# Optimization experiments

Measured on AMD Instinct MI355X. Metric: run time of the kernel, lower is better.

Reference implementation:

```python
import jax, jax.numpy as jnp
import numpy as np

B, T, D_IN, H = 256, 512, 64, 128
S_MIN, S_FRAC = 0.5, 0.5


def _gru_cell(x_i, h, W_ih, W_hh, b_ih, b_hh):
    # torch.nn.GRUCell semantics
    gi = x_i @ W_ih.T + b_ih          # [B, 3H]
    gh = h @ W_hh.T + b_hh            # [B, 3H]
    i_r, i_z, i_n = jnp.split(gi, 3, axis=-1)
    h_r, h_z, h_n = jnp.split(gh, 3, axis=-1)
    r = jax.nn.sigmoid(i_r + h_r)
    z = jax.nn.sigmoid(i_z + h_z)
    n = jnp.tanh(i_n + r * h_n)
    return (1.0 - z) * n + z * h


def _rk4_step(h, dt, W_node, b_node):
    # one fixed RK4 step of dh/dt = tanh(h @ W_node^T + b_node) over [t, t+dt]
    f = lambda hh: jnp.tanh(hh @ W_node.T + b_node)
    k1 = f(h)
    k2 = f(h + 0.5 * dt * k1)
    k3 = f(h + 0.5 * dt * k2)
    k4 = f(h + dt * k3)
    return h + (dt / 6.0) * (k1 + 2.0 * k2 + 2.0 * k3 + k4)


def setup_inputs() -> dict:
    key = jax.random.key(0)
    ks = jax.random.split(key, 8)
    x = jax.random.normal(ks[0], (B, T, D_IN), dtype=jnp.float32)
    # sorted per-sample time grid; all lens == T so argmax-longest picks row 0
    tp = jnp.broadcast_to(jnp.linspace(0.01, 1.0, T, dtype=jnp.float32), (B, T))
    # generate_samp_mask(x, s_min=0.5, s_frac=0.5), deterministic seed
    rng = np.random.default_rng(0)
    minimum_ind = int(T * S_MIN)
    extrap_ind = int(rng.integers(minimum_ind, T))
    n_inds = int(S_FRAC * extrap_ind)
    samp_inds = np.sort(rng.choice(np.arange(extrap_ind), n_inds, replace=False))
    mask_np = np.zeros(T, dtype=bool)
    mask_np[samp_inds] = True
    samp_mask = jnp.asarray(mask_np)
    s = 1.0 / np.sqrt(H)
    W_ih = jax.random.uniform(ks[1], (3 * H, D_IN), jnp.float32, -s, s)
    W_hh = jax.random.uniform(ks[2], (3 * H, H), jnp.float32, -s, s)
    b_ih = jax.random.uniform(ks[3], (3 * H,), jnp.float32, -s, s)
    b_hh = jax.random.uniform(ks[4], (3 * H,), jnp.float32, -s, s)
    W_node = jax.random.normal(ks[5], (H, H), jnp.float32) * 0.05
    b_node = jnp.zeros((H,), jnp.float32)
    W_out = jax.random.uniform(ks[6], (D_IN, H), jnp.float32, -s, s)
    b_out = jax.random.uniform(ks[7], (D_IN,), jnp.float32, -s, s)
    return {"x": x, "tp": tp, "samp_mask": samp_mask,
            "W_ih": W_ih, "W_hh": W_hh, "b_ih": b_ih, "b_hh": b_hh,
            "W_node": W_node, "b_node": b_node, "W_out": W_out, "b_out": b_out}


def reference(x, tp, samp_mask, W_ih, W_hh, b_ih, b_hh, W_node, b_node, W_out, b_out):
    # get_longest_tp: all lens equal -> row 0; prepend tp[0]-0.01
    t0 = tp[0]                                   # [T]
    ts = jnp.concatenate([t0[:1] - 0.01, t0])    # [T+1]
    dts = ts[1:] - ts[:-1]                       # [T]
    xs = jnp.transpose(x, (1, 0, 2))             # [T, B, D_in]
    h0 = jnp.zeros((x.shape[0], W_hh.shape[1]), x.dtype)

    def step(h, inp):
        dt, x_i, use_x = inp
        h_ode = _rk4_step(h, dt, W_node, b_node)
        prev_out = h @ W_out.T + b_out           # teacher-forcing from own output
        inp_vec = jnp.where(use_x, x_i, prev_out)
        h_new = _gru_cell(inp_vec, h_ode, W_ih, W_hh, b_ih, b_hh)
        return h_new, h_new

    _, h_arr = jax.lax.scan(step, h0, (dts, xs, samp_mask))  # [T, B, H]
    h_arr = jnp.transpose(h_arr, (1, 0, 2))                  # [B, T, H]
    out = h_arr @ W_out.T + b_out                            # [B, T, D_in]
    # select_by_length with all lens == T -> flat [B*T, D_in]
    return out.reshape(-1, out.shape[-1])
```

## Files before the change

kernel.cpp:

```cpp
#include <hip/hip_runtime.h>


#define NB    256
#define TB    512
#define TSTEP 512
#define DIN   64
#define HD    128

typedef float v2f __attribute__((ext_vector_type(2)));

__device__ __forceinline__ float fast_tanh(float v) {
    float e = __expf(2.0f * v);
    return 1.0f - 2.0f / (e + 1.0f);
}
__device__ __forceinline__ float fast_sigmoid(float v) {
    return 1.0f / (1.0f + __expf(-v));
}

__device__ __forceinline__ float quad_red(float v) {
    v += __int_as_float(__builtin_amdgcn_update_dpp(
            0, __float_as_int(v), 0xB1, 0xF, 0xF, true));
    v += __int_as_float(__builtin_amdgcn_update_dpp(
            0, __float_as_int(v), 0x4E, 0xF, 0xF, true));
    return v;
}

__global__ __launch_bounds__(TB, 2) void gruode_kernel(
    const float* __restrict__ x,
    const float* __restrict__ tp,
    const int*   __restrict__ samp_mask,
    const float* __restrict__ W_ih,
    const float* __restrict__ W_hh,
    const float* __restrict__ b_ih,
    const float* __restrict__ b_hh,
    const float* __restrict__ W_node,
    const float* __restrict__ b_node,
    const float* __restrict__ W_out,
    const float* __restrict__ b_out,
    float*       __restrict__ out)
{
    const int t   = threadIdx.x;
    const int b   = blockIdx.x;
    const int j   = t >> 2;
    const int kq  = t & 3;
    const int j64 = t >> 3;
    const int ko  = t & 7;

    __shared__ __align__(16) float sh_h [HD];
    __shared__ __align__(16) float sh_t0[HD];
    __shared__ __align__(16) float sh_t1[HD];
    __shared__ __align__(16) float sh_in[DIN];
    __shared__ __align__(16) float sh_po[DIN];

    const float4* Wn4  = (const float4*)W_node;
    const float4* Whh4 = (const float4*)W_hh;
    const float4* Wih4 = (const float4*)W_ih;
    const float4* Wo4  = (const float4*)W_out;

    v2f Wn[16], Whr[16], Whz[16], Whn[16];
    #pragma unroll
    for (int i = 0; i < 8; ++i) {
        float4 w;
        w = Wn4 [j*32 + i*4 + kq];          Wn [2*i] = (v2f){w.x, w.y}; Wn [2*i+1] = (v2f){w.z, w.w};
        w = Whh4[(0*HD + j)*32 + i*4 + kq]; Whr[2*i] = (v2f){w.x, w.y}; Whr[2*i+1] = (v2f){w.z, w.w};
        w = Whh4[(1*HD + j)*32 + i*4 + kq]; Whz[2*i] = (v2f){w.x, w.y}; Whz[2*i+1] = (v2f){w.z, w.w};
        w = Whh4[(2*HD + j)*32 + i*4 + kq]; Whn[2*i] = (v2f){w.x, w.y}; Whn[2*i+1] = (v2f){w.z, w.w};
    }
    v2f Wir[8], Wiz[8], Win[8], Wo[8];
    #pragma unroll
    for (int i = 0; i < 4; ++i) {
        float4 w;
        w = Wih4[(0*HD + j)*16 + i*4 + kq]; Wir[2*i] = (v2f){w.x, w.y}; Wir[2*i+1] = (v2f){w.z, w.w};
        w = Wih4[(1*HD + j)*16 + i*4 + kq]; Wiz[2*i] = (v2f){w.x, w.y}; Wiz[2*i+1] = (v2f){w.z, w.w};
        w = Wih4[(2*HD + j)*16 + i*4 + kq]; Win[2*i] = (v2f){w.x, w.y}; Win[2*i+1] = (v2f){w.z, w.w};
        w = Wo4 [j64*32 + i*8 + ko];        Wo [2*i] = (v2f){w.x, w.y}; Wo [2*i+1] = (v2f){w.z, w.w};
    }
    #pragma unroll
    for (int i = 0; i < 16; ++i) {
        asm volatile("" : "+v"(Wn[i]));  asm volatile("" : "+v"(Whr[i]));
        asm volatile("" : "+v"(Whz[i])); asm volatile("" : "+v"(Whn[i]));
    }
    #pragma unroll
    for (int i = 0; i < 8; ++i) {
        asm volatile("" : "+v"(Wir[i])); asm volatile("" : "+v"(Wiz[i]));
        asm volatile("" : "+v"(Win[i])); asm volatile("" : "+v"(Wo[i]));
    }

    const float bn   = b_node[j];
    const float br   = b_ih[0*HD + j] + b_hh[0*HD + j];
    const float bz   = b_ih[1*HD + j] + b_hh[1*HD + j];
    const float bi_n = b_ih[2*HD + j];
    const float bh_n = b_hh[2*HD + j];
    const float bo   = b_out[j64];

    if (t < HD)  sh_h[t]  = 0.0f;
    if (t < DIN) sh_po[t] = b_out[t];

    float tp_cur  = tp[0];
    float tp_prev = tp_cur - 0.01f;
    int   m_cur   = samp_mask[0];
    float xr = (t < DIN) ? x[(size_t)b * TSTEP * DIN + t] : 0.0f;

    __syncthreads();

    const float4* h4  = (const float4*)sh_h;
    const float4* t04 = (const float4*)sh_t0;
    const float4* t14 = (const float4*)sh_t1;
    const float4* in4 = (const float4*)sh_in;

    auto hdot = [&](const v2f (&w)[16], const float4* buf) -> float {
        v2f a0 = {0.f, 0.f}, a1 = {0.f, 0.f};
        #pragma unroll
        for (int i = 0; i < 8; ++i) {
            float4 v = buf[i*4 + kq];
            a0 += w[2*i]   * (v2f){v.x, v.y};
            a1 += w[2*i+1] * (v2f){v.z, v.w};
        }
        v2f a = a0 + a1;
        return a.x + a.y;
    };

    float hj = 0.0f;

    #pragma unroll 1
    for (int s = 0; s < TSTEP; ++s) {
        const float dt = tp_cur - tp_prev;

        if (t < DIN) sh_in[t] = m_cur ? xr : sh_po[t];

        {
            const int sn = (s + 1 < TSTEP) ? s + 1 : s;
            tp_prev = tp_cur;
            tp_cur  = tp[sn];
            m_cur   = samp_mask[sn];
            if (t < DIN) xr = x[((size_t)b * TSTEP + sn) * DIN + t];
        }

        float k1 = fast_tanh(quad_red(hdot(Wn, h4)) + bn);
        if (kq == 0) sh_t0[j] = fmaf(0.5f * dt, k1, hj);
        __syncthreads();

        float k2 = fast_tanh(quad_red(hdot(Wn, t04)) + bn);
        if (kq == 0) sh_t1[j] = fmaf(0.5f * dt, k2, hj);
        __syncthreads();

        float k3 = fast_tanh(quad_red(hdot(Wn, t14)) + bn);
        if (kq == 0) sh_t0[j] = fmaf(dt, k3, hj);
        __syncthreads();

        float k4 = fast_tanh(quad_red(hdot(Wn, t04)) + bn);
        float hode = fmaf(dt * (1.0f / 6.0f),
                          (k1 + 2.0f * k2) + (2.0f * k3 + k4), hj);
        if (kq == 0) sh_t1[j] = hode;
        __syncthreads();

        v2f ar = {0.f,0.f}, az = {0.f,0.f}, an = {0.f,0.f};
        #pragma unroll
        for (int i = 0; i < 8; ++i) {
            float4 v = t14[i*4 + kq];
            v2f lo = {v.x, v.y}, hi = {v.z, v.w};
            ar += Whr[2*i] * lo; ar += Whr[2*i+1] * hi;
            az += Whz[2*i] * lo; az += Whz[2*i+1] * hi;
            an += Whn[2*i] * lo; an += Whn[2*i+1] * hi;
        }
        v2f cr = {0.f,0.f}, cz = {0.f,0.f}, cn = {0.f,0.f};
        #pragma unroll
        for (int i = 0; i < 4; ++i) {
            float4 v = in4[i*4 + kq];
            v2f lo = {v.x, v.y}, hi = {v.z, v.w};
            cr += Wir[2*i] * lo; cr += Wir[2*i+1] * hi;
            cz += Wiz[2*i] * lo; cz += Wiz[2*i+1] * hi;
            cn += Win[2*i] * lo; cn += Win[2*i+1] * hi;
        }
        float rr  = fast_sigmoid(quad_red((ar.x + ar.y) + (cr.x + cr.y)) + br);
        float zz  = fast_sigmoid(quad_red((az.x + az.y) + (cz.x + cz.y)) + bz);
        float hnv = quad_red(an.x + an.y) + bh_n;
        float inv = quad_red(cn.x + cn.y) + bi_n;
        float nn  = fast_tanh(fmaf(rr, hnv, inv));
        float hnew = fmaf(zz, hode - nn, nn);
        hj = hnew;

        if (kq == 0) sh_h[j] = hnew;
        __syncthreads();

        v2f ao = {0.f, 0.f};
        #pragma unroll
        for (int i = 0; i < 4; ++i) {
            float4 v = h4[i*8 + ko];
            ao += Wo[2*i]   * (v2f){v.x, v.y};
            ao += Wo[2*i+1] * (v2f){v.z, v.w};
        }
        float o = quad_red(ao.x + ao.y);
        o += __shfl_xor(o, 4);
        o += bo;
        if (ko == 0) {
            sh_po[j64] = o;
            out[((size_t)b * TSTEP + s) * DIN + j64] = o;
        }
        __syncthreads();
    }
}

extern "C" void kernel_launch(void* const* d_in, const int* in_sizes, int n_in,
                              void* d_out, int out_size, void* d_ws, size_t ws_size,
                              hipStream_t stream) {
    (void)in_sizes; (void)n_in; (void)d_ws; (void)ws_size; (void)out_size;
    const float* x      = (const float*)d_in[0];
    const float* tp     = (const float*)d_in[1];
    const int*   mask   = (const int*)  d_in[2];
    const float* W_ih   = (const float*)d_in[3];
    const float* W_hh   = (const float*)d_in[4];
    const float* b_ih   = (const float*)d_in[5];
    const float* b_hh   = (const float*)d_in[6];
    const float* W_node = (const float*)d_in[7];
    const float* b_node = (const float*)d_in[8];
    const float* W_out  = (const float*)d_in[9];
    const float* b_out  = (const float*)d_in[10];
    float* outp = (float*)d_out;

    gruode_kernel<<<NB, TB, 0, stream>>>(x, tp, mask, W_ih, W_hh, b_ih, b_hh,
                                         W_node, b_node, W_out, b_out, outp);
}
```

Before: 1.227 ms.

## Double threads per block, fuse output projection into RK4 stage, cut barriers

Raises the block size to 1024 threads with eight threads per hidden unit, so each thread holds half as many weights and the per-thread dot products are shorter. W_ih moves from registers into padded shared memory, and its input-side GRU products are computed during the RK4 stages. The output projection of the previous hidden state is folded into the k1 stage, which removes one barrier per timestep. The trade-offs are wider reductions using ds_swizzle, extra shared-memory reads of W_ih, and possibly lower occupancy per CU.

```diff
diff --git a/kernel.cpp b/kernel.cpp
--- a/kernel.cpp
+++ b/kernel.cpp
@@ -1,11 +1,12 @@
 #include <hip/hip_runtime.h>
 
 
-#define NB    256
-#define TB    512
-#define TSTEP 512
-#define DIN   64
-#define HD    128
+#define NB      256
+#define TB      1024
+#define TSTEP   512
+#define DIN     64
+#define HD      128
+#define WIH_PAD 17
 
 typedef float v2f __attribute__((ext_vector_type(2)));
 
@@ -17,15 +18,21 @@
     return 1.0f / (1.0f + __expf(-v));
 }
 
-__device__ __forceinline__ float quad_red(float v) {
+__device__ __forceinline__ float red8(float v) {
     v += __int_as_float(__builtin_amdgcn_update_dpp(
             0, __float_as_int(v), 0xB1, 0xF, 0xF, true));
     v += __int_as_float(__builtin_amdgcn_update_dpp(
             0, __float_as_int(v), 0x4E, 0xF, 0xF, true));
+    v += __int_as_float(__builtin_amdgcn_ds_swizzle(__float_as_int(v), 0x101F));
     return v;
 }
-
-__global__ __launch_bounds__(TB, 2) void gruode_kernel(
+__device__ __forceinline__ float red16(float v) {
+    v = red8(v);
+    v += __int_as_float(__builtin_amdgcn_ds_swizzle(__float_as_int(v), 0x201F));
+    return v;
+}
+
+__global__ __launch_bounds__(TB, 4) void gruode_kernel(
     const float* __restrict__ x,
     const float* __restrict__ tp,
     const int*   __restrict__ samp_mask,
@@ -41,50 +48,50 @@
 {
     const int t   = threadIdx.x;
     const int b   = blockIdx.x;
-    const int j   = t >> 2;
-    const int kq  = t & 3;
-    const int j64 = t >> 3;
-    const int ko  = t & 7;
+    const int j   = t >> 3;
+    const int ks  = t & 7;
+    const int j64 = t >> 4;
+    const int ko  = t & 15;
 
     __shared__ __align__(16) float sh_h [HD];
     __shared__ __align__(16) float sh_t0[HD];
     __shared__ __align__(16) float sh_t1[HD];
     __shared__ __align__(16) float sh_in[DIN];
     __shared__ __align__(16) float sh_po[DIN];
+    __shared__ float4 sWih[3 * HD * WIH_PAD];
 
     const float4* Wn4  = (const float4*)W_node;
     const float4* Whh4 = (const float4*)W_hh;
     const float4* Wih4 = (const float4*)W_ih;
     const float4* Wo4  = (const float4*)W_out;
 
-    v2f Wn[16], Whr[16], Whz[16], Whn[16];
-    #pragma unroll
-    for (int i = 0; i < 8; ++i) {
-        float4 w;
-        w = Wn4 [j*32 + i*4 + kq];          Wn [2*i] = (v2f){w.x, w.y}; Wn [2*i+1] = (v2f){w.z, w.w};
-        w = Whh4[(0*HD + j)*32 + i*4 + kq]; Whr[2*i] = (v2f){w.x, w.y}; Whr[2*i+1] = (v2f){w.z, w.w};
-        w = Whh4[(1*HD + j)*32 + i*4 + kq]; Whz[2*i] = (v2f){w.x, w.y}; Whz[2*i+1] = (v2f){w.z, w.w};
-        w = Whh4[(2*HD + j)*32 + i*4 + kq]; Whn[2*i] = (v2f){w.x, w.y}; Whn[2*i+1] = (v2f){w.z, w.w};
-    }
-    v2f Wir[8], Wiz[8], Win[8], Wo[8];
+    for (int idx = t; idx < 3 * HD * 16; idx += TB) {
+        int row = idx >> 4, col = idx & 15;
+        sWih[row * WIH_PAD + col] = Wih4[idx];
+    }
+
+    v2f Wn[8], Whr[8], Whz[8], Whn[8];
     #pragma unroll
     for (int i = 0; i < 4; ++i) {
         float4 w;
-        w = Wih4[(0*HD + j)*16 + i*4 + kq]; Wir[2*i] = (v2f){w.x, w.y}; Wir[2*i+1] = (v2f){w.z, w.w};
-        w = Wih4[(1*HD + j)*16 + i*4 + kq]; Wiz[2*i] = (v2f){w.x, w.y}; Wiz[2*i+1] = (v2f){w.z, w.w};
-        w = Wih4[(2*HD + j)*16 + i*4 + kq]; Win[2*i] = (v2f){w.x, w.y}; Win[2*i+1] = (v2f){w.z, w.w};
-        w = Wo4 [j64*32 + i*8 + ko];        Wo [2*i] = (v2f){w.x, w.y}; Wo [2*i+1] = (v2f){w.z, w.w};
-    }
-    #pragma unroll
-    for (int i = 0; i < 16; ++i) {
+        w = Wn4 [j*32 + i*8 + ks];          Wn [2*i] = (v2f){w.x, w.y}; Wn [2*i+1] = (v2f){w.z, w.w};
+        w = Whh4[(0*HD + j)*32 + i*8 + ks]; Whr[2*i] = (v2f){w.x, w.y}; Whr[2*i+1] = (v2f){w.z, w.w};
+        w = Whh4[(1*HD + j)*32 + i*8 + ks]; Whz[2*i] = (v2f){w.x, w.y}; Whz[2*i+1] = (v2f){w.z, w.w};
+        w = Whh4[(2*HD + j)*32 + i*8 + ks]; Whn[2*i] = (v2f){w.x, w.y}; Whn[2*i+1] = (v2f){w.z, w.w};
+    }
+    v2f Wo[4];
+    #pragma unroll
+    for (int i = 0; i < 2; ++i) {
+        float4 w = Wo4[j64*32 + i*16 + ko];
+        Wo[2*i] = (v2f){w.x, w.y}; Wo[2*i+1] = (v2f){w.z, w.w};
+    }
+    #pragma unroll
+    for (int i = 0; i < 8; ++i) {
         asm volatile("" : "+v"(Wn[i]));  asm volatile("" : "+v"(Whr[i]));
         asm volatile("" : "+v"(Whz[i])); asm volatile("" : "+v"(Whn[i]));
     }
     #pragma unroll
-    for (int i = 0; i < 8; ++i) {
-        asm volatile("" : "+v"(Wir[i])); asm volatile("" : "+v"(Wiz[i]));
-        asm volatile("" : "+v"(Win[i])); asm volatile("" : "+v"(Wo[i]));
-    }
+    for (int i = 0; i < 4; ++i) { asm volatile("" : "+v"(Wo[i])); }
 
     const float bn   = b_node[j];
     const float br   = b_ih[0*HD + j] + b_hh[0*HD + j];
@@ -93,13 +100,14 @@
     const float bh_n = b_hh[2*HD + j];
     const float bo   = b_out[j64];
 
-    if (t < HD)  sh_h[t]  = 0.0f;
-    if (t < DIN) sh_po[t] = b_out[t];
+    if (t < HD) sh_h[t] = 0.0f;
 
     float tp_cur  = tp[0];
     float tp_prev = tp_cur - 0.01f;
     int   m_cur   = samp_mask[0];
-    float xr = (t < DIN) ? x[(size_t)b * TSTEP * DIN + t] : 0.0f;
+    const float* xbase = x   + (size_t)b * TSTEP * DIN;
+    float*       obase = out + (size_t)b * TSTEP * DIN;
+    float xr = (t < DIN) ? xbase[t] : 0.0f;
 
     __syncthreads();
 
@@ -108,11 +116,11 @@
     const float4* t14 = (const float4*)sh_t1;
     const float4* in4 = (const float4*)sh_in;
 
-    auto hdot = [&](const v2f (&w)[16], const float4* buf) -> float {
+    auto hdot = [&](const v2f (&w)[8], const float4* buf) -> float {
         v2f a0 = {0.f, 0.f}, a1 = {0.f, 0.f};
         #pragma unroll
-        for (int i = 0; i < 8; ++i) {
-            float4 v = buf[i*4 + kq];
+        for (int i = 0; i < 4; ++i) {
+            float4 v = buf[i*8 + ks];
             a0 += w[2*i]   * (v2f){v.x, v.y};
             a1 += w[2*i+1] * (v2f){v.z, v.w};
         }
@@ -126,78 +134,94 @@
     for (int s = 0; s < TSTEP; ++s) {
         const float dt = tp_cur - tp_prev;
 
+        float k1 = fast_tanh(red8(hdot(Wn, h4)) + bn);
+        {
+            v2f ao = {0.f, 0.f};
+            #pragma unroll
+            for (int i = 0; i < 2; ++i) {
+                float4 v = h4[i*16 + ko];
+                ao += Wo[2*i]   * (v2f){v.x, v.y};
+                ao += Wo[2*i+1] * (v2f){v.z, v.w};
+            }
+            float o = red16(ao.x + ao.y) + bo;
+            if (ko == 0) {
+                sh_po[j64] = o;
+                if (s > 0) obase[(size_t)(s-1) * DIN + j64] = o;
+            }
+        }
+        if (ks == 0) sh_t0[j] = fmaf(0.5f * dt, k1, hj);
+        __syncthreads();
+
         if (t < DIN) sh_in[t] = m_cur ? xr : sh_po[t];
-
+        float k2 = fast_tanh(red8(hdot(Wn, t04)) + bn);
+        if (ks == 0) sh_t1[j] = fmaf(0.5f * dt, k2, hj);
         {
             const int sn = (s + 1 < TSTEP) ? s + 1 : s;
             tp_prev = tp_cur;
             tp_cur  = tp[sn];
             m_cur   = samp_mask[sn];
-            if (t < DIN) xr = x[((size_t)b * TSTEP + sn) * DIN + t];
-        }
-
-        float k1 = fast_tanh(quad_red(hdot(Wn, h4)) + bn);
-        if (kq == 0) sh_t0[j] = fmaf(0.5f * dt, k1, hj);
-        __syncthreads();
-
-        float k2 = fast_tanh(quad_red(hdot(Wn, t04)) + bn);
-        if (kq == 0) sh_t1[j] = fmaf(0.5f * dt, k2, hj);
-        __syncthreads();
-
-        float k3 = fast_tanh(quad_red(hdot(Wn, t14)) + bn);
-        if (kq == 0) sh_t0[j] = fmaf(dt, k3, hj);
-        __syncthreads();
-
-        float k4 = fast_tanh(quad_red(hdot(Wn, t04)) + bn);
+            if (t < DIN) xr = xbase[(size_t)sn * DIN + t];
+        }
+        __syncthreads();
+
+        float k3 = fast_tanh(red8(hdot(Wn, t14)) + bn);
+        float crs, czs, cns;
+        {
+            v2f cr = {0.f,0.f}, cz = {0.f,0.f}, cn = {0.f,0.f};
+            #pragma unroll
+            for (int i = 0; i < 2; ++i) {
+                float4 v = in4[i*8 + ks];
+                v2f lo = {v.x, v.y}, hi = {v.z, v.w};
+                float4 wr = sWih[(0*HD + j)*WIH_PAD + i*8 + ks];
+                float4 wz = sWih[(1*HD + j)*WIH_PAD + i*8 + ks];
+                float4 wn = sWih[(2*HD + j)*WIH_PAD + i*8 + ks];
+                cr += (v2f){wr.x, wr.y} * lo; cr += (v2f){wr.z, wr.w} * hi;
+                cz += (v2f){wz.x, wz.y} * lo; cz += (v2f){wz.z, wz.w} * hi;
+                cn += (v2f){wn.x, wn.y} * lo; cn += (v2f){wn.z, wn.w} * hi;
+            }
+            crs = red8(cr.x + cr.y);
+            czs = red8(cz.x + cz.y);
+            cns = red8(cn.x + cn.y);
+        }
+        if (ks == 0) sh_t0[j] = fmaf(dt, k3, hj);
+        __syncthreads();
+
+        float k4 = fast_tanh(red8(hdot(Wn, t04)) + bn);
         float hode = fmaf(dt * (1.0f / 6.0f),
                           (k1 + 2.0f * k2) + (2.0f * k3 + k4), hj);
-        if (kq == 0) sh_t1[j] = hode;
+        if (ks == 0) sh_t1[j] = hode;
         __syncthreads();
 
         v2f ar = {0.f,0.f}, az = {0.f,0.f}, an = {0.f,0.f};
         #pragma unroll
-        for (int i = 0; i < 8; ++i) {
-            float4 v = t14[i*4 + kq];
+        for (int i = 0; i < 4; ++i) {
+            float4 v = t14[i*8 + ks];
             v2f lo = {v.x, v.y}, hi = {v.z, v.w};
             ar += Whr[2*i] * lo; ar += Whr[2*i+1] * hi;
             az += Whz[2*i] * lo; az += Whz[2*i+1] * hi;
             an += Whn[2*i] * lo; an += Whn[2*i+1] * hi;
         }
-        v2f cr = {0.f,0.f}, cz = {0.f,0.f}, cn = {0.f,0.f};
-        #pragma unroll
-        for (int i = 0; i < 4; ++i) {
-            float4 v = in4[i*4 + kq];
-            v2f lo = {v.x, v.y}, hi = {v.z, v.w};
-            cr += Wir[2*i] * lo; cr += Wir[2*i+1] * hi;
-            cz += Wiz[2*i] * lo; cz += Wiz[2*i+1] * hi;
-            cn += Win[2*i] * lo; cn += Win[2*i+1] * hi;
-        }
-        float rr  = fast_sigmoid(quad_red((ar.x + ar.y) + (cr.x + cr.y)) + br);
-        float zz  = fast_sigmoid(quad_red((az.x + az.y) + (cz.x + cz.y)) + bz);
-        float hnv = quad_red(an.x + an.y) + bh_n;
-        float inv = quad_red(cn.x + cn.y) + bi_n;
+        float rr  = fast_sigmoid(red8(ar.x + ar.y) + crs + br);
+        float zz  = fast_sigmoid(red8(az.x + az.y) + czs + bz);
+        float hnv = red8(an.x + an.y) + bh_n;
+        float inv = cns + bi_n;
         float nn  = fast_tanh(fmaf(rr, hnv, inv));
         float hnew = fmaf(zz, hode - nn, nn);
         hj = hnew;
-
-        if (kq == 0) sh_h[j] = hnew;
-        __syncthreads();
-
+        if (ks == 0) sh_h[j] = hnew;
+        __syncthreads();
+    }
+
+    {
         v2f ao = {0.f, 0.f};
         #pragma unroll
-        for (int i = 0; i < 4; ++i) {
-            float4 v = h4[i*8 + ko];
+        for (int i = 0; i < 2; ++i) {
+            float4 v = h4[i*16 + ko];
             ao += Wo[2*i]   * (v2f){v.x, v.y};
             ao += Wo[2*i+1] * (v2f){v.z, v.w};
         }
-        float o = quad_red(ao.x + ao.y);
-        o += __shfl_xor(o, 4);
-        o += bo;
-        if (ko == 0) {
-            sh_po[j64] = o;
-            out[((size_t)b * TSTEP + s) * DIN + j64] = o;
-        }
-        __syncthreads();
+        float o = red16(ao.x + ao.y) + bo;
+        if (ko == 0) obase[(size_t)(TSTEP - 1) * DIN + j64] = o;
     }
 }
 
```

Result: slower. 1.617 ms (+31.8%).
